# Kernel optimization log

Hardware: AMD Instinct MI355X
Metric: run time of the kernel (lower is better)

The kernel has to match this reference:

```python
import jax, jax.numpy as jnp
import numpy as np

D_MODEL, D_FF, N_EXP, TOP_K = 1024, 4096, 8, 2


def setup_inputs() -> dict:
    key = jax.random.key(0)
    ks = jax.random.split(key, 8)
    s = 1.0 / np.sqrt(D_MODEL)
    sf = 1.0 / np.sqrt(D_FF)
    return {
        "x": jax.random.normal(ks[0], (2, 2048, D_MODEL), dtype=jnp.float32),
        "Wr": jax.random.uniform(ks[1], (D_MODEL, N_EXP), minval=-s, maxval=s, dtype=jnp.float32),
        "br": jnp.zeros((N_EXP,), jnp.float32),
        "W1": jax.random.uniform(ks[2], (N_EXP, D_MODEL, D_FF), minval=-s, maxval=s, dtype=jnp.float32),
        "b1": jnp.zeros((N_EXP, D_FF), jnp.float32),
        "W2": jax.random.uniform(ks[3], (N_EXP, D_FF, D_MODEL), minval=-sf, maxval=sf, dtype=jnp.float32),
        "b2": jnp.zeros((N_EXP, D_MODEL), jnp.float32),
    }


def _moe(x, Wr, br, W1, b1, W2, b2):
    B, S, D = x.shape
    xf = x.reshape(-1, D)                               # [T, D]
    logits = xf @ Wr + br                               # [T, E] router logits
    probs = jax.nn.softmax(logits, axis=-1)
    top_vals, top_idx = jax.lax.top_k(probs, TOP_K)     # [T, K]
    gates = top_vals / jnp.sum(top_vals, axis=-1, keepdims=True)
    # dense all-expert FFN (clean reference for the masked gather/scatter loop)
    h = jax.nn.gelu(jnp.einsum('td,edf->etf', xf, W1) + b1[:, None, :], approximate=False)
    y = jnp.einsum('etf,efd->etd', h, W2) + b2[:, None, :]   # [E, T, D]
    # combine weights per (token, expert): sum_k gate_k * onehot(idx_k)
    w_te = jnp.sum(jax.nn.one_hot(top_idx, N_EXP, dtype=x.dtype) * gates[..., None], axis=1)  # [T, E]
    out = jnp.einsum('te,etd->td', w_te, y)
    return out.reshape(B, S, D)


def reference(x, Wr, br, W1, b1, W2, b2):
    return _moe(x, Wr, br, W1, b1, W2, b2)
```

## Files before the change

### kernel.cpp

```cpp
#include <hip/hip_runtime.h>
#include <hip/hip_bf16.h>

#define T_TOK 4096
#define DMODEL 1024
#define DFF 4096
#define NEXP 8
#define ROWS_TOT 8192
#define ROWS_PAD 8448

typedef __bf16 bf16x8 __attribute__((ext_vector_type(8)));
typedef float f32x4 __attribute__((ext_vector_type(4)));
typedef unsigned short u16;

template<int V> struct ic { static constexpr int value = V; };

__device__ __forceinline__ u16 f2bf(float f) {
    __hip_bfloat16 b = __float2bfloat16(f);
    return __builtin_bit_cast(u16, b);
}
__device__ __forceinline__ float bf2f(u16 u) {
    unsigned v = (unsigned)u << 16;
    return __builtin_bit_cast(float, v);
}

__device__ __forceinline__ float fast_gelu(float v) {
    const float x = v * 0.70710678118654752f;
    const float ax = fabsf(x);
    const float t = 1.f / fmaf(0.3275911f, ax, 1.f);
    float p = fmaf(1.061405429f, t, -1.453152027f);
    p = fmaf(p, t, 1.421413741f);
    p = fmaf(p, t, -0.284496736f);
    p = fmaf(p, t, 0.254829592f);
    p *= t;
    const float e = __expf(-ax * ax);
    float erfv = fmaf(-p, e, 1.f);
    erfv = copysignf(erfv, x);
    return 0.5f * v * (1.f + erfv);
}

__global__ void router_kernel(const float* __restrict__ x, const float* __restrict__ Wr,
                              const float* __restrict__ br, int* __restrict__ top_idx,
                              float* __restrict__ gates, int* __restrict__ counts) {
    const int t = blockIdx.x;
    const int lane = threadIdx.x;
    float part[8];
#pragma unroll
    for (int e = 0; e < 8; ++e) part[e] = 0.f;
#pragma unroll
    for (int j = 0; j < 4; ++j) {
        const int d0 = j * 256 + lane * 4;
        const float4 xv = *(const float4*)(x + (size_t)t * DMODEL + d0);
        const float xs[4] = {xv.x, xv.y, xv.z, xv.w};
#pragma unroll
        for (int i = 0; i < 4; ++i) {
            const float4 w0 = *(const float4*)(Wr + (d0 + i) * 8);
            const float4 w1 = *(const float4*)(Wr + (d0 + i) * 8 + 4);
            part[0] += xs[i] * w0.x; part[1] += xs[i] * w0.y;
            part[2] += xs[i] * w0.z; part[3] += xs[i] * w0.w;
            part[4] += xs[i] * w1.x; part[5] += xs[i] * w1.y;
            part[6] += xs[i] * w1.z; part[7] += xs[i] * w1.w;
        }
    }
#pragma unroll
    for (int m = 32; m > 0; m >>= 1)
#pragma unroll
        for (int e = 0; e < 8; ++e) part[e] += __shfl_xor(part[e], m, 64);
    if (lane == 0) {
        float l[8];
#pragma unroll
        for (int e = 0; e < 8; ++e) l[e] = part[e] + br[e];
        int i1 = 0;
#pragma unroll
        for (int e = 1; e < 8; ++e) if (l[e] > l[i1]) i1 = e;
        int i2 = (i1 == 0) ? 1 : 0;
#pragma unroll
        for (int e = 0; e < 8; ++e) if (e != i1 && l[e] > l[i2]) i2 = e;
        const float e2 = expf(l[i2] - l[i1]);
        const float inv = 1.f / (1.f + e2);
        top_idx[t * 2 + 0] = i1;  gates[t * 2 + 0] = inv;
        top_idx[t * 2 + 1] = i2;  gates[t * 2 + 1] = e2 * inv;
        atomicAdd(&counts[i1], 1);
        atomicAdd(&counts[i2], 1);
    }
}

__global__ void fillscan_kernel(const int* __restrict__ top_idx, const int* __restrict__ counts,
                                int* __restrict__ offs, int* __restrict__ rowtoken,
                                int* __restrict__ slotof) {
    __shared__ int lcur[8];
    if (threadIdx.x == 0) {
        int s = 0;
        for (int e = 0; e < 8; ++e) { offs[e] = s; lcur[e] = s; s += counts[e]; }
        offs[8] = s;
    }
    __syncthreads();
    for (int t = threadIdx.x; t < T_TOK; t += 1024) {
#pragma unroll
        for (int k = 0; k < 2; ++k) {
            const int e = top_idx[t * 2 + k];
            const int p = atomicAdd(&lcur[e], 1);
            rowtoken[p] = t;
            slotof[t * 2 + k] = p;
        }
    }
}

__global__ void gather_kernel(const float* __restrict__ x, const int* __restrict__ rowtoken,
                              u16* __restrict__ Xg) {
    const int p = blockIdx.x;
    const int t = rowtoken[p];
    const int d = threadIdx.x * 4;
    const float4 v = *(const float4*)(x + (size_t)t * DMODEL + d);
    ushort4 o;
    o.x = f2bf(v.x); o.y = f2bf(v.y); o.z = f2bf(v.z); o.w = f2bf(v.w);
    *(ushort4*)(Xg + (size_t)p * DMODEL + d) = o;
}

__global__ __launch_bounds__(256) void transpose_convert_kernel(
    const float* __restrict__ src, u16* __restrict__ dst, int R, int C) {
    __shared__ float tile[64][65];
    const size_t base = (size_t)blockIdx.z * R * C;
    const int r0 = blockIdx.y * 64, c0 = blockIdx.x * 64;
    const int tr = threadIdx.x >> 4;
    const int tc4 = (threadIdx.x & 15) * 4;
#pragma unroll
    for (int i = 0; i < 4; ++i) {
        const int r = tr + i * 16;
        const float4 v = *(const float4*)(src + base + (size_t)(r0 + r) * C + c0 + tc4);
        tile[r][tc4 + 0] = v.x; tile[r][tc4 + 1] = v.y;
        tile[r][tc4 + 2] = v.z; tile[r][tc4 + 3] = v.w;
    }
    __syncthreads();
#pragma unroll
    for (int i = 0; i < 4; ++i) {
        const int rr = tr + i * 16;
        ushort4 o;
        o.x = f2bf(tile[tc4 + 0][rr]);
        o.y = f2bf(tile[tc4 + 1][rr]);
        o.z = f2bf(tile[tc4 + 2][rr]);
        o.w = f2bf(tile[tc4 + 3][rr]);
        *(ushort4*)(dst + base + (size_t)(c0 + rr) * R + r0 + tc4) = o;
    }
}

template<bool GELU>
__global__ __launch_bounds__(512, 2) void gemm8ph_kernel(
    const u16* __restrict__ Amat, const int lda,
    const u16* __restrict__ Bmat, const int ldb,
    const float* __restrict__ bias,
    u16* __restrict__ C0, u16* __restrict__ C1, const int ldc,
    const int* __restrict__ offs, const int* __restrict__ counts,
    const int Ntot, const int NT, const int KH, const int J, const int GM) {
    int bid = blockIdx.x;
    const int e  = bid & 7;   bid >>= 3;
    const int kh = bid % KH;  bid /= KH;
    const int tn = bid % NT;  bid /= NT;
    const int tm0 = bid;
    const int cnt = counts[e];
    if (tm0 * 256 >= cnt) return;
    const int pend  = offs[e] + cnt;
    const int nbase = tn * 256;
    const int k0 = kh * (J << 6);
    u16* __restrict__ Cmat = kh ? C1 : C0;

    __shared__ __align__(16) u16 As[2][2][128 * 64];
    __shared__ __align__(16) u16 Bs[2][2][128 * 64];

    const int tid = threadIdx.x;
    const int lane = tid & 63, wid = tid >> 6;
    const int wr = (wid >> 2) * 64;
    const int wc = (wid & 3) * 32;
    const int fr = lane & 15, fg = lane >> 4;
    const int rsw = (fr & 7) * 8;

    const int srow = tid >> 3;
    const int scol = 8 * ((tid & 7) ^ ((tid >> 3) & 7));
    const u16* Bpt = Bmat + (size_t)e * Ntot * ldb
                          + (size_t)(nbase + srow) * ldb + k0 + scol;

    float bv[2][2];
#pragma unroll
    for (int q = 0; q < 2; ++q)
#pragma unroll
        for (int n = 0; n < 2; ++n)
            bv[q][n] = GELU ? bias[e * Ntot + nbase + q * 128 + wc + n * 16 + fr] : 0.f;

    for (int tm = tm0; tm * 256 < cnt; tm += GM) {
        const int pbase = offs[e] + tm * 256;
        const u16* Apt = Amat + (size_t)(pbase + srow) * lda + k0 + scol;

        f32x4 acc[2][2][4][2];
#pragma unroll
        for (int qm = 0; qm < 2; ++qm)
#pragma unroll
            for (int qn = 0; qn < 2; ++qn)
#pragma unroll
                for (int m = 0; m < 4; ++m)
#pragma unroll
                    for (int n = 0; n < 2; ++n)
                        acc[qm][qn][m][n] = (f32x4){0.f, 0.f, 0.f, 0.f};

        bf16x8 aA[4][2];
        bf16x8 bB[2][2][2];

        auto stageHalf = [&](int tile, int which) {
            const int b = tile & 1;
            const int kofs = tile << 6;
            if ((which & 1) == 0) {
                const int h = which >> 1;
#pragma unroll
                for (int i = 0; i < 2; ++i)
                    __builtin_amdgcn_global_load_lds(
                        (const __attribute__((address_space(1))) void*)
                            (Apt + kofs + (size_t)(h * 128 + 64 * i) * lda),
                        (__attribute__((address_space(3))) void*)(&As[b][h][(size_t)(tid + 512 * i) * 8]),
                        16, 0, 0);
            } else {
                const int h = which >> 1;
#pragma unroll
                for (int i = 0; i < 2; ++i)
                    __builtin_amdgcn_global_load_lds(
                        (const __attribute__((address_space(1))) void*)
                            (Bpt + kofs + (size_t)(h * 128 + 64 * i) * ldb),
                        (__attribute__((address_space(3))) void*)(&Bs[b][h][(size_t)(tid + 512 * i) * 8]),
                        16, 0, 0);
            }
        };

        __syncthreads();
#pragma unroll
        for (int q = 0; q < 4; ++q) stageHalf(0, q);
#pragma unroll
        for (int q = 0; q < 4; ++q) stageHalf(1, q);

        int phi = 0;
        const int smax = 4 * (J - 2);
        auto phase = [&](auto BBc, auto QMc, auto QNc, auto RDAc, auto RDBc) {
            constexpr int BB  = decltype(BBc)::value;
            constexpr int QM  = decltype(QMc)::value;
            constexpr int QN  = decltype(QNc)::value;
            constexpr int RDA = decltype(RDAc)::value;
            constexpr int RDB = decltype(RDBc)::value;
            asm volatile("s_waitcnt vmcnt(6)" ::: "memory");
            __builtin_amdgcn_s_barrier();
            asm volatile("" ::: "memory");
            if constexpr (RDA) {
#pragma unroll
                for (int m = 0; m < 4; ++m)
#pragma unroll
                    for (int kc = 0; kc < 2; ++kc)
                        aA[m][kc] = *(const bf16x8*)(&As[BB][QM][
                            (wr + m * 16 + fr) * 64 + ((kc * 32 + fg * 8) ^ rsw)]);
            }
            if constexpr (RDB >= 0) {
#pragma unroll
                for (int n = 0; n < 2; ++n)
#pragma unroll
                    for (int kc = 0; kc < 2; ++kc)
                        bB[RDB][n][kc] = *(const bf16x8*)(&Bs[BB][RDB][
                            (wc + n * 16 + fr) * 64 + ((kc * 32 + fg * 8) ^ rsw)]);
            }
            {
                const int s = phi - 1;
                if (s >= 0 && s < smax) {
                    constexpr int sord[4] = {0, 1, 3, 2};
                    stageHalf(2 + (s >> 2), sord[s & 3]);
                }
                ++phi;
            }
            __builtin_amdgcn_s_setprio(1);
#pragma unroll
            for (int kc = 0; kc < 2; ++kc)
#pragma unroll
                for (int m = 0; m < 4; ++m)
#pragma unroll
                    for (int n = 0; n < 2; ++n)
                        acc[QM][QN][m][n] = __builtin_amdgcn_mfma_f32_16x16x32_bf16(
                            aA[m][kc], bB[QN][n][kc], acc[QM][QN][m][n], 0, 0, 0);
            __builtin_amdgcn_s_setprio(0);
        };

        const int niter = J >> 1;
        for (int it = 0; it < niter; ++it) {
            phase(ic<0>{}, ic<0>{}, ic<0>{}, ic<1>{}, ic<0>{});
            phase(ic<0>{}, ic<0>{}, ic<1>{}, ic<0>{}, ic<1>{});
            phase(ic<0>{}, ic<1>{}, ic<1>{}, ic<1>{}, ic<-1>{});
            phase(ic<0>{}, ic<1>{}, ic<0>{}, ic<0>{}, ic<-1>{});
            phase(ic<1>{}, ic<0>{}, ic<0>{}, ic<1>{}, ic<0>{});
            phase(ic<1>{}, ic<0>{}, ic<1>{}, ic<0>{}, ic<1>{});
            phase(ic<1>{}, ic<1>{}, ic<1>{}, ic<1>{}, ic<-1>{});
            phase(ic<1>{}, ic<1>{}, ic<0>{}, ic<0>{}, ic<-1>{});
        }

#pragma unroll
        for (int qm = 0; qm < 2; ++qm) {
#pragma unroll
            for (int m = 0; m < 4; ++m) {
#pragma unroll
                for (int r = 0; r < 4; ++r) {
                    const int p = pbase + qm * 128 + wr + m * 16 + fg * 4 + r;
                    if (p >= pend) continue;
#pragma unroll
                    for (int qn = 0; qn < 2; ++qn) {
#pragma unroll
                        for (int n = 0; n < 2; ++n) {
                            const int col = nbase + qn * 128 + wc + n * 16 + fr;
                            float v = acc[qm][qn][m][n][r];
                            if (GELU) v = fast_gelu(v + bv[qn][n]);
                            Cmat[(size_t)p * ldc + col] = f2bf(v);
                        }
                    }
                }
            }
        }
    }
}

__global__ void combine_kernel(const u16* __restrict__ ybuf0, const u16* __restrict__ ybuf1,
                               const float* __restrict__ b2,
                               const int* __restrict__ top_idx, const float* __restrict__ gates,
                               const int* __restrict__ slotof, float* __restrict__ out) {
    const int t = blockIdx.x;
    const int d = threadIdx.x * 4;
    const int e0 = top_idx[t * 2 + 0], e1 = top_idx[t * 2 + 1];
    const float g0 = gates[t * 2 + 0], g1 = gates[t * 2 + 1];
    const int p0 = slotof[t * 2 + 0], p1 = slotof[t * 2 + 1];
    const ushort4 ya0 = *(const ushort4*)(ybuf0 + (size_t)p0 * DMODEL + d);
    const ushort4 ya1 = *(const ushort4*)(ybuf1 + (size_t)p0 * DMODEL + d);
    const ushort4 yb0 = *(const ushort4*)(ybuf0 + (size_t)p1 * DMODEL + d);
    const ushort4 yb1 = *(const ushort4*)(ybuf1 + (size_t)p1 * DMODEL + d);
    const float4 ba = *(const float4*)(b2 + e0 * DMODEL + d);
    const float4 bb = *(const float4*)(b2 + e1 * DMODEL + d);
    float4 o;
    o.x = g0 * (bf2f(ya0.x) + bf2f(ya1.x) + ba.x) + g1 * (bf2f(yb0.x) + bf2f(yb1.x) + bb.x);
    o.y = g0 * (bf2f(ya0.y) + bf2f(ya1.y) + ba.y) + g1 * (bf2f(yb0.y) + bf2f(yb1.y) + bb.y);
    o.z = g0 * (bf2f(ya0.z) + bf2f(ya1.z) + ba.z) + g1 * (bf2f(yb0.z) + bf2f(yb1.z) + bb.z);
    o.w = g0 * (bf2f(ya0.w) + bf2f(ya1.w) + ba.w) + g1 * (bf2f(yb0.w) + bf2f(yb1.w) + bb.w);
    *(float4*)(out + (size_t)t * DMODEL + d) = o;
}

extern "C" void kernel_launch(void* const* d_in, const int* in_sizes, int n_in,
                              void* d_out, int out_size, void* d_ws, size_t ws_size,
                              hipStream_t stream) {
    const float* x  = (const float*)d_in[0];
    const float* Wr = (const float*)d_in[1];
    const float* br = (const float*)d_in[2];
    const float* W1 = (const float*)d_in[3];
    const float* b1 = (const float*)d_in[4];
    const float* W2 = (const float*)d_in[5];
    const float* b2 = (const float*)d_in[6];
    float* out = (float*)d_out;

    char* w = (char*)d_ws;
    int*   counts   = (int*)(w + 0);
    int*   offs     = (int*)(w + 64);
    int*   top_idx  = (int*)(w + 1024);
    float* gates    = (float*)(w + 1024 + 32768);
    int*   rowtoken = (int*)(w + 1024 + 65536);
    int*   slotof   = (int*)(w + 1024 + 65536 + 40960);
    u16*   Xg       = (u16*)(w + 1024 + 65536 + 40960 + 32768);
    u16*   hbuf     = Xg + (size_t)ROWS_PAD * DMODEL;
    u16*   W1T      = hbuf + (size_t)ROWS_PAD * DFF;
    u16*   W2T      = W1T + (size_t)NEXP * DFF * DMODEL;
    u16*   ybuf0    = Xg;
    u16*   ybuf1    = W1T;
    const size_t need = (size_t)(1024 + 65536 + 40960 + 32768)
        + (size_t)ROWS_PAD * DMODEL * 2 + (size_t)ROWS_PAD * DFF * 2
        + (size_t)NEXP * DFF * DMODEL * 4;
    if (ws_size < need) return;

    hipMemsetAsync(d_ws, 0, 64, stream);

    transpose_convert_kernel<<<dim3(64, 16, 8), 256, 0, stream>>>(W1, W1T, DMODEL, DFF);
    transpose_convert_kernel<<<dim3(16, 64, 8), 256, 0, stream>>>(W2, W2T, DFF, DMODEL);

    router_kernel<<<T_TOK, 64, 0, stream>>>(x, Wr, br, top_idx, gates, counts);
    fillscan_kernel<<<1, 1024, 0, stream>>>(top_idx, counts, offs, rowtoken, slotof);
    gather_kernel<<<ROWS_TOT, 256, 0, stream>>>(x, rowtoken, Xg);

    gemm8ph_kernel<true><<<768, 512, 0, stream>>>(
        Xg, DMODEL, W1T, DMODEL, b1, hbuf, nullptr, DFF,
        offs, counts, DFF, 16, 1, 16, 6);
    gemm8ph_kernel<false><<<384, 512, 0, stream>>>(
        hbuf, DFF, W2T, DFF, nullptr, ybuf0, ybuf1, DMODEL,
        offs, counts, DMODEL, 4, 2, 32, 6);
    combine_kernel<<<T_TOK, 256, 0, stream>>>(ybuf0, ybuf1, b2, top_idx, gates, slotof, out);
}
```

Before: 441.2 us.

## Templatize grouped GEMM dimensions and rewrite the staged MFMA pipeline schedule

Makes K, N and the K-split compile-time template parameters so strides, tile counts and loop trip counts are constants. Replaces the generic phase lambda, which used a runtime stage counter, with an explicitly unrolled two-tile loop. That loop interleaves LDS reads, global-to-LDS prefetches and MFMA blocks, with extra barriers around each MFMA group and waitcnt points that change at the tail. The aim is less address and branch overhead and tighter copy/compute overlap, at the cost of more barriers per iteration.

```diff
diff --git a/kernel.cpp b/kernel.cpp
--- a/kernel.cpp
+++ b/kernel.cpp
@@ -11,8 +11,6 @@
 typedef __bf16 bf16x8 __attribute__((ext_vector_type(8)));
 typedef float f32x4 __attribute__((ext_vector_type(4)));
 typedef unsigned short u16;
-
-template<int V> struct ic { static constexpr int value = V; };
 
 __device__ __forceinline__ u16 f2bf(float f) {
     __hip_bfloat16 b = __float2bfloat16(f);
@@ -143,14 +141,16 @@
     }
 }
 
-template<bool GELU>
+template<int KTOT, int NTOT, int KH, bool GELU>
 __global__ __launch_bounds__(512, 2) void gemm8ph_kernel(
-    const u16* __restrict__ Amat, const int lda,
-    const u16* __restrict__ Bmat, const int ldb,
+    const u16* __restrict__ Amat, const u16* __restrict__ Bmat,
     const float* __restrict__ bias,
-    u16* __restrict__ C0, u16* __restrict__ C1, const int ldc,
-    const int* __restrict__ offs, const int* __restrict__ counts,
-    const int Ntot, const int NT, const int KH, const int J, const int GM) {
+    u16* __restrict__ C0, u16* __restrict__ C1,
+    const int* __restrict__ offs, const int* __restrict__ counts) {
+    constexpr int J  = KTOT / (KH * 64);
+    constexpr int NT = NTOT / 256;
+    constexpr int GM = 6;
+
     int bid = blockIdx.x;
     const int e  = bid & 7;   bid >>= 3;
     const int kh = bid % KH;  bid /= KH;
@@ -160,7 +160,7 @@
     if (tm0 * 256 >= cnt) return;
     const int pend  = offs[e] + cnt;
     const int nbase = tn * 256;
-    const int k0 = kh * (J << 6);
+    const int k0 = kh * (J * 64);
     u16* __restrict__ Cmat = kh ? C1 : C0;
 
     __shared__ __align__(16) u16 As[2][2][128 * 64];
@@ -175,19 +175,19 @@
 
     const int srow = tid >> 3;
     const int scol = 8 * ((tid & 7) ^ ((tid >> 3) & 7));
-    const u16* Bpt = Bmat + (size_t)e * Ntot * ldb
-                          + (size_t)(nbase + srow) * ldb + k0 + scol;
+    const u16* Bpt = Bmat + (size_t)e * NTOT * KTOT
+                          + (size_t)(nbase + srow) * KTOT + k0 + scol;
 
     float bv[2][2];
 #pragma unroll
     for (int q = 0; q < 2; ++q)
 #pragma unroll
         for (int n = 0; n < 2; ++n)
-            bv[q][n] = GELU ? bias[e * Ntot + nbase + q * 128 + wc + n * 16 + fr] : 0.f;
+            bv[q][n] = GELU ? bias[e * NTOT + nbase + q * 128 + wc + n * 16 + fr] : 0.f;
 
     for (int tm = tm0; tm * 256 < cnt; tm += GM) {
         const int pbase = offs[e] + tm * 256;
-        const u16* Apt = Amat + (size_t)(pbase + srow) * lda + k0 + scol;
+        const u16* Apt = Amat + (size_t)(pbase + srow) * KTOT + k0 + scol;
 
         f32x4 acc[2][2][4][2];
 #pragma unroll
@@ -200,96 +200,98 @@
                     for (int n = 0; n < 2; ++n)
                         acc[qm][qn][m][n] = (f32x4){0.f, 0.f, 0.f, 0.f};
 
-        bf16x8 aA[4][2];
-        bf16x8 bB[2][2][2];
-
-        auto stageHalf = [&](int tile, int which) {
-            const int b = tile & 1;
-            const int kofs = tile << 6;
-            if ((which & 1) == 0) {
-                const int h = which >> 1;
-#pragma unroll
-                for (int i = 0; i < 2; ++i)
-                    __builtin_amdgcn_global_load_lds(
-                        (const __attribute__((address_space(1))) void*)
-                            (Apt + kofs + (size_t)(h * 128 + 64 * i) * lda),
-                        (__attribute__((address_space(3))) void*)(&As[b][h][(size_t)(tid + 512 * i) * 8]),
-                        16, 0, 0);
-            } else {
-                const int h = which >> 1;
-#pragma unroll
-                for (int i = 0; i < 2; ++i)
-                    __builtin_amdgcn_global_load_lds(
-                        (const __attribute__((address_space(1))) void*)
-                            (Bpt + kofs + (size_t)(h * 128 + 64 * i) * ldb),
-                        (__attribute__((address_space(3))) void*)(&Bs[b][h][(size_t)(tid + 512 * i) * 8]),
-                        16, 0, 0);
-            }
-        };
-
-        __syncthreads();
-#pragma unroll
-        for (int q = 0; q < 4; ++q) stageHalf(0, q);
-#pragma unroll
-        for (int q = 0; q < 4; ++q) stageHalf(1, q);
-
-        int phi = 0;
-        const int smax = 4 * (J - 2);
-        auto phase = [&](auto BBc, auto QMc, auto QNc, auto RDAc, auto RDBc) {
-            constexpr int BB  = decltype(BBc)::value;
-            constexpr int QM  = decltype(QMc)::value;
-            constexpr int QN  = decltype(QNc)::value;
-            constexpr int RDA = decltype(RDAc)::value;
-            constexpr int RDB = decltype(RDBc)::value;
-            asm volatile("s_waitcnt vmcnt(6)" ::: "memory");
+        bf16x8 aA[4][2], bB0[2][2], bB1[2][2];
+
+        auto stgA = [&](int buf, int h, int tile) {
+#pragma unroll
+            for (int i = 0; i < 2; ++i)
+                __builtin_amdgcn_global_load_lds(
+                    (const __attribute__((address_space(1))) void*)
+                        (Apt + ((size_t)tile << 6) + (size_t)(h * 128 + 64 * i) * KTOT),
+                    (__attribute__((address_space(3))) void*)(&As[buf][h][(size_t)(tid + 512 * i) * 8]),
+                    16, 0, 0);
+        };
+        auto stgB = [&](int buf, int h, int tile) {
+#pragma unroll
+            for (int i = 0; i < 2; ++i)
+                __builtin_amdgcn_global_load_lds(
+                    (const __attribute__((address_space(1))) void*)
+                        (Bpt + ((size_t)tile << 6) + (size_t)(h * 128 + 64 * i) * KTOT),
+                    (__attribute__((address_space(3))) void*)(&Bs[buf][h][(size_t)(tid + 512 * i) * 8]),
+                    16, 0, 0);
+        };
+        auto rdA = [&](int buf, int h) {
+#pragma unroll
+            for (int m = 0; m < 4; ++m)
+#pragma unroll
+                for (int kc = 0; kc < 2; ++kc)
+                    aA[m][kc] = *(const bf16x8*)(&As[buf][h][
+                        (wr + m * 16 + fr) * 64 + ((kc * 32 + fg * 8) ^ rsw)]);
+        };
+        auto rdB = [&](bf16x8 (&dst)[2][2], int buf, int h) {
+#pragma unroll
+            for (int n = 0; n < 2; ++n)
+#pragma unroll
+                for (int kc = 0; kc < 2; ++kc)
+                    dst[n][kc] = *(const bf16x8*)(&Bs[buf][h][
+                        (wc + n * 16 + fr) * 64 + ((kc * 32 + fg * 8) ^ rsw)]);
+        };
+        auto mma = [&](int qm, int qn, bf16x8 (&bb)[2][2]) {
+            __builtin_amdgcn_s_setprio(1);
+#pragma unroll
+            for (int kc = 0; kc < 2; ++kc)
+#pragma unroll
+                for (int m = 0; m < 4; ++m)
+#pragma unroll
+                    for (int n = 0; n < 2; ++n)
+                        acc[qm][qn][m][n] = __builtin_amdgcn_mfma_f32_16x16x32_bf16(
+                            aA[m][kc], bb[n][kc], acc[qm][qn][m][n], 0, 0, 0);
+            __builtin_amdgcn_s_setprio(0);
+        };
+        auto bar = [&]() {
+            asm volatile("" ::: "memory");
             __builtin_amdgcn_s_barrier();
             asm volatile("" ::: "memory");
-            if constexpr (RDA) {
-#pragma unroll
-                for (int m = 0; m < 4; ++m)
-#pragma unroll
-                    for (int kc = 0; kc < 2; ++kc)
-                        aA[m][kc] = *(const bf16x8*)(&As[BB][QM][
-                            (wr + m * 16 + fr) * 64 + ((kc * 32 + fg * 8) ^ rsw)]);
-            }
-            if constexpr (RDB >= 0) {
-#pragma unroll
-                for (int n = 0; n < 2; ++n)
-#pragma unroll
-                    for (int kc = 0; kc < 2; ++kc)
-                        bB[RDB][n][kc] = *(const bf16x8*)(&Bs[BB][RDB][
-                            (wc + n * 16 + fr) * 64 + ((kc * 32 + fg * 8) ^ rsw)]);
-            }
-            {
-                const int s = phi - 1;
-                if (s >= 0 && s < smax) {
-                    constexpr int sord[4] = {0, 1, 3, 2};
-                    stageHalf(2 + (s >> 2), sord[s & 3]);
-                }
-                ++phi;
-            }
-            __builtin_amdgcn_s_setprio(1);
-#pragma unroll
-            for (int kc = 0; kc < 2; ++kc)
-#pragma unroll
-                for (int m = 0; m < 4; ++m)
-#pragma unroll
-                    for (int n = 0; n < 2; ++n)
-                        acc[QM][QN][m][n] = __builtin_amdgcn_mfma_f32_16x16x32_bf16(
-                            aA[m][kc], bB[QN][n][kc], acc[QM][QN][m][n], 0, 0, 0);
-            __builtin_amdgcn_s_setprio(0);
-        };
-
-        const int niter = J >> 1;
-        for (int it = 0; it < niter; ++it) {
-            phase(ic<0>{}, ic<0>{}, ic<0>{}, ic<1>{}, ic<0>{});
-            phase(ic<0>{}, ic<0>{}, ic<1>{}, ic<0>{}, ic<1>{});
-            phase(ic<0>{}, ic<1>{}, ic<1>{}, ic<1>{}, ic<-1>{});
-            phase(ic<0>{}, ic<1>{}, ic<0>{}, ic<0>{}, ic<-1>{});
-            phase(ic<1>{}, ic<0>{}, ic<0>{}, ic<1>{}, ic<0>{});
-            phase(ic<1>{}, ic<0>{}, ic<1>{}, ic<0>{}, ic<1>{});
-            phase(ic<1>{}, ic<1>{}, ic<1>{}, ic<1>{}, ic<-1>{});
-            phase(ic<1>{}, ic<1>{}, ic<0>{}, ic<0>{}, ic<-1>{});
+        };
+
+        stgA(0, 0, 0); stgB(0, 0, 0); stgB(0, 1, 0); stgA(0, 1, 0);
+        stgA(1, 0, 1); stgB(1, 0, 1); stgB(1, 1, 1);
+        asm volatile("s_waitcnt vmcnt(6)" ::: "memory");
+        bar();
+
+#pragma unroll 1
+        for (int it2 = 0; it2 < J / 2; ++it2) {
+            const int cur = it2 * 2;
+            const bool s2 = (cur + 2 < J);
+            const bool s3 = (cur + 3 < J);
+            rdA(0, 0); rdB(bB0, 0, 0);
+            stgA(1, 1, cur + 1);
+            bar(); mma(0, 0, bB0); bar();
+            rdB(bB1, 0, 1);
+            if (s2) stgA(0, 0, cur + 2);
+            bar(); mma(0, 1, bB1); bar();
+            rdA(0, 1);
+            if (s2) stgB(0, 0, cur + 2);
+            bar(); mma(1, 1, bB1); bar();
+            if (s2) stgB(0, 1, cur + 2);
+            bar(); mma(1, 0, bB0);
+            if (s2) asm volatile("s_waitcnt vmcnt(6)" ::: "memory");
+            else    asm volatile("s_waitcnt vmcnt(0)" ::: "memory");
+            bar();
+            rdA(1, 0); rdB(bB0, 1, 0);
+            if (s2) stgA(0, 1, cur + 2);
+            bar(); mma(0, 0, bB0); bar();
+            rdB(bB1, 1, 1);
+            if (s3) stgA(1, 0, cur + 3);
+            bar(); mma(0, 1, bB1); bar();
+            rdA(1, 1);
+            if (s3) stgB(1, 0, cur + 3);
+            bar(); mma(1, 1, bB1); bar();
+            if (s3) stgB(1, 1, cur + 3);
+            bar(); mma(1, 0, bB0);
+            if (s3) asm volatile("s_waitcnt vmcnt(6)" ::: "memory");
+            else    asm volatile("s_waitcnt vmcnt(0)" ::: "memory");
+            bar();
         }
 
 #pragma unroll
@@ -307,7 +309,7 @@
                             const int col = nbase + qn * 128 + wc + n * 16 + fr;
                             float v = acc[qm][qn][m][n][r];
                             if (GELU) v = fast_gelu(v + bv[qn][n]);
-                            Cmat[(size_t)p * ldc + col] = f2bf(v);
+                            Cmat[(size_t)p * NTOT + col] = f2bf(v);
                         }
                     }
                 }
@@ -378,11 +380,9 @@
     fillscan_kernel<<<1, 1024, 0, stream>>>(top_idx, counts, offs, rowtoken, slotof);
     gather_kernel<<<ROWS_TOT, 256, 0, stream>>>(x, rowtoken, Xg);
 
-    gemm8ph_kernel<true><<<768, 512, 0, stream>>>(
-        Xg, DMODEL, W1T, DMODEL, b1, hbuf, nullptr, DFF,
-        offs, counts, DFF, 16, 1, 16, 6);
-    gemm8ph_kernel<false><<<384, 512, 0, stream>>>(
-        hbuf, DFF, W2T, DFF, nullptr, ybuf0, ybuf1, DMODEL,
-        offs, counts, DMODEL, 4, 2, 32, 6);
+    gemm8ph_kernel<1024, 4096, 1, true><<<768, 512, 0, stream>>>(
+        Xg, W1T, b1, hbuf, nullptr, offs, counts);
+    gemm8ph_kernel<4096, 1024, 2, false><<<384, 512, 0, stream>>>(
+        hbuf, W2T, nullptr, ybuf0, ybuf1, offs, counts);
     combine_kernel<<<T_TOK, 256, 0, stream>>>(ybuf0, ybuf1, b2, top_idx, gates, slotof, out);
 }
```

Measured after the change: 444.1 us. About the same (+0.7%).
